# Performance work log

Measured on AMD Instinct MI355X. Metric: run time of the kernel, lower is better.

The kernel has to match this reference:

```python
import jax, jax.numpy as jnp
import numpy as np

B, T, D, H, C = 32, 512, 768, 512, 7


def setup_inputs() -> dict:
    key = jax.random.key(0)
    ks = jax.random.split(key, 10)
    g = lambda k, shape: jax.random.normal(k, shape, jnp.float32) * 0.02
    return {
        "x": jax.random.normal(ks[0], (B, T, D), jnp.float32),
        # PyTorch LSTM params; b = b_ih + b_hh folded into one bias (same math)
        "Wf_ih": g(ks[1], (4 * H, 2 * D)),
        "Wf_hh": g(ks[2], (4 * H, H)),
        "bf": jnp.zeros((4 * H,), jnp.float32),
        "Wb_ih": g(ks[3], (4 * H, 2 * D)),
        "Wb_hh": g(ks[4], (4 * H, H)),
        "bb": jnp.zeros((4 * H,), jnp.float32),
        "W_enc": g(ks[5], (H, D)),
        "b_enc": jnp.zeros((H,), jnp.float32),
        "W_dec": g(ks[6], (H, H)),
        "b_dec": jnp.zeros((H,), jnp.float32),
        "v": jax.random.uniform(ks[7], (H,), jnpp := jnp.float32) if False else jax.random.uniform(ks[7], (H,), jnp.float32),
        "W_head": g(ks[8], (C, 2 * H)),
        "b_head": jnp.zeros((C,), jnp.float32),
    }


def reference(x, Wf_ih, Wf_hh, bf, Wb_ih, Wb_hh, bb, W_enc, b_enc, W_dec, b_dec, v, W_head, b_head):
    hid = W_dec.shape[0]
    # encoder projection is time-invariant -> hoist out of the loop (same math as original)
    enc_proj = jnp.einsum('btd,hd->bth', x, W_enc) + b_enc  # (B,T,H)

    def run_direction(x_seq, Wih, Whh, b):
        def step(carry, xt):
            h, c = carry                                    # (B,H) each
            dec = h @ W_dec.T + b_dec                       # (B,H)
            scores = jnp.tanh(enc_proj + dec[:, None, :]) @ v  # (B,T)
            w = jax.nn.softmax(scores, axis=1)
            ctx = jnp.einsum('bt,btd->bd', w, x)            # (B,D)
            inp = jnp.concatenate([ctx, xt], axis=1)        # (B,2D)
            gates = inp @ Wih.T + h @ Whh.T + b             # (B,4H), torch order i,f,g,o
            i_, f_, g_, o_ = jnp.split(gates, 4, axis=1)
            c = jax.nn.sigmoid(f_) * c + jax.nn.sigmoid(i_) * jnp.tanh(g_)
            h = jax.nn.sigmoid(o_) * jnp.tanh(c)
            return (h, c), h

        h0 = jnp.zeros((x.shape[0], hid), x.dtype)
        (_, _), hs = jax.lax.scan(step, (h0, h0), x_seq)
        return hs                                           # (T,B,H)

    x_seq = jnp.swapaxes(x, 0, 1)                           # (T,B,D)
    hs_f = run_direction(x_seq, Wf_ih, Wf_hh, bf)
    hs_b = run_direction(x_seq[::-1], Wb_ih, Wb_hh, bb)[::-1]
    comb = jnp.swapaxes(jnp.concatenate([hs_f, hs_b], axis=-1), 0, 1)  # (B,T,2H)
    return comb @ W_head.T + b_head                          # (B,T,C)
```

## Files before the change

kernel.cpp:

```cpp
#include <hip/hip_runtime.h>
#include <cstdint>
#include <cstddef>

#define L2E 1.4426950408889634f

typedef __attribute__((ext_vector_type(8))) short short8v;
typedef __attribute__((ext_vector_type(4))) float f32x4;
typedef unsigned long long ull;

__device__ __forceinline__ float fexp2(float x){ return __builtin_amdgcn_exp2f(x); }
__device__ __forceinline__ float frcp(float x){ return __builtin_amdgcn_rcpf(x); }
__device__ __forceinline__ float tanh_f(float x){
  return 1.f - 2.f*frcp(1.f + fexp2(2.f*L2E*x));
}
__device__ __forceinline__ float sigm_f(float x){
  return frcp(1.f + fexp2(-L2E*x));
}
__device__ __forceinline__ float bf2f(ushort u){ return __uint_as_float(((uint32_t)u)<<16); }
__device__ __forceinline__ ushort f2bf(float f){
  uint32_t x = __float_as_uint(f);
  uint32_t r = (x + 0x7FFFu + ((x>>16)&1u)) >> 16;
  return (ushort)r;
}

__device__ __forceinline__ float ld4f(const float* p){
  return __hip_atomic_load((float*)p, __ATOMIC_RELAXED, __HIP_MEMORY_SCOPE_AGENT);
}
__device__ __forceinline__ void st4f(float* p, float v){
  __hip_atomic_store(p, v, __ATOMIC_RELAXED, __HIP_MEMORY_SCOPE_AGENT);
}
__device__ __forceinline__ void st2h(ushort* p, ushort v){
  __hip_atomic_store(p, v, __ATOMIC_RELAXED, __HIP_MEMORY_SCOPE_AGENT);
}
__device__ __forceinline__ short8v ld16h(const ushort* p){
  union { ull u[2]; short8v s; } c;
  c.u[0] = __hip_atomic_load((ull*)p,     __ATOMIC_RELAXED, __HIP_MEMORY_SCOPE_AGENT);
  c.u[1] = __hip_atomic_load((ull*)(p+4), __ATOMIC_RELAXED, __HIP_MEMORY_SCOPE_AGENT);
  return c.s;
}
__device__ __forceinline__ void st8u(ushort* p, ull v){
  __hip_atomic_store((ull*)p, v, __ATOMIC_RELAXED, __HIP_MEMORY_SCOPE_AGENT);
}

namespace {
constexpr int NB = 32, TT = 512, DD = 768, HH = 512;
constexpr size_t EPB  = 0;
constexpr size_t XBB  = EPB  + (size_t)NB*HH*TT*2;
constexpr size_t HSB  = XBB  + (size_t)NB*TT*DD*2;
constexpr size_t WPKB = HSB  + (size_t)2*TT*NB*HH*2;
constexpr size_t WDPB = WPKB + (size_t)2*128*64*64*8*2;
constexpr size_t UCTXB= WDPB + (size_t)32*16*64*8*2;
constexpr size_t ZBB  = UCTXB+ (size_t)2*NB*DD*4;
constexpr size_t DECB = ZBB  + (size_t)2*NB*4;
constexpr size_t CSTB = DECB + (size_t)2*NB*HH*4;
constexpr size_t GSYB = CSTB + (size_t)2*NB*HH*4;
constexpr size_t WS_BYTES = GSYB + 32768;

constexpr int EPL  = 0;
constexpr int WPL  = 65536;
constexpr int REDL = 131072;
constexpr int HEVL = 147456;
constexpr int DPL  = 151552;
constexpr int DECL = 153600;
constexpr int VVL  = 154112;
constexpr int CSCL = 154368;
constexpr int GFNL = 157440;
constexpr int LDS_BYTES = GFNL + 2176;
}

__device__ __forceinline__ void bar_arrive(uint* flags, uint token, int bid){
  __syncthreads();
  if (threadIdx.x == 0)
    __hip_atomic_store(&flags[bid*16], token, __ATOMIC_RELAXED, __HIP_MEMORY_SCOPE_AGENT);
}
__device__ __forceinline__ void bar_wait(uint* flags, uint token){
  if (threadIdx.x < 64) {
    #pragma unroll
    for (int j = 0; j < 4; j++) {
      while (__hip_atomic_load(&flags[(threadIdx.x*4 + j)*16], __ATOMIC_RELAXED, __HIP_MEMORY_SCOPE_AGENT) < token)
        __builtin_amdgcn_s_sleep(1);
    }
  }
  __syncthreads();
  asm volatile("" ::: "memory");
}

__global__ void k_xcast(const float* __restrict__ x, ushort* __restrict__ xb)
{
  size_t i = ((size_t)blockIdx.x*256 + threadIdx.x)*8;
  float4 v0 = *(const float4*)(x + i);
  float4 v1 = *(const float4*)(x + i + 4);
  short8v o;
  o[0]=(short)f2bf(v0.x); o[1]=(short)f2bf(v0.y); o[2]=(short)f2bf(v0.z); o[3]=(short)f2bf(v0.w);
  o[4]=(short)f2bf(v1.x); o[5]=(short)f2bf(v1.y); o[6]=(short)f2bf(v1.z); o[7]=(short)f2bf(v1.w);
  *(short8v*)(xb + i) = o;
}

__global__ void k_encproj(const float* __restrict__ x, const float* __restrict__ Wenc,
                          const float* __restrict__ benc, ushort* __restrict__ epT)
{
  int b = blockIdx.z, h0 = blockIdx.y*64, t0 = blockIdx.x*64;
  __shared__ float As[64][33];
  __shared__ float Bs[64][33];
  int tid = threadIdx.x;
  int n = tid & 63, mg = tid >> 6;
  float acc[16];
  #pragma unroll
  for (int j = 0; j < 16; j++) acc[j] = 0.f;
  int lr = tid >> 2, lk = (tid & 3) * 8;
  for (int k0 = 0; k0 < 768; k0 += 32) {
    const float* ap = Wenc + (size_t)(h0 + lr)*768 + k0 + lk;
    #pragma unroll
    for (int i = 0; i < 8; i++) As[lr][lk + i] = ap[i];
    const float* bp = x + ((size_t)b*512 + t0 + lr)*768 + k0 + lk;
    #pragma unroll
    for (int i = 0; i < 8; i++) Bs[lr][lk + i] = bp[i];
    __syncthreads();
    #pragma unroll
    for (int kk = 0; kk < 32; kk++) {
      float bv = Bs[n][kk];
      #pragma unroll
      for (int j = 0; j < 16; j++) acc[j] += As[mg*16 + j][kk] * bv;
    }
    __syncthreads();
  }
  #pragma unroll
  for (int j = 0; j < 16; j++) {
    int h = h0 + mg*16 + j;
    epT[((size_t)b*512 + h)*512 + t0 + n] = f2bf(acc[j] + benc[h]);
  }
}

__global__ void k_wpack(const float* __restrict__ Wfih, const float* __restrict__ Wfhh,
                        const float* __restrict__ Wbih, const float* __restrict__ Wbhh,
                        ushort* __restrict__ wpk)
{
  size_t f = (size_t)blockIdx.x*256 + threadIdx.x;
  int lane = (int)(f & 63), kstep = (int)((f>>6)&63), jblk = (int)((f>>12)&127), dir = (int)(f>>19);
  const float* Whh = dir ? Wbhh : Wfhh;
  const float* Wih = dir ? Wbih : Wfih;
  int c = lane & 15, gate = c >> 2, jj = c & 3;
  int row = gate*512 + jblk*4 + jj;
  int kbase = kstep*32 + (lane>>4)*8;
  short8v o;
  #pragma unroll
  for (int i = 0; i < 8; i++) {
    int k = kbase + i;
    float w = (k < 512) ? Whh[(size_t)row*512 + k] : Wih[(size_t)row*1536 + (k - 512)];
    o[i] = (short)f2bf(w);
  }
  *(short8v*)(wpk + f*8) = o;
}

__global__ void k_wdpack(const float* __restrict__ Wdec, ushort* __restrict__ wdp)
{
  int f = blockIdx.x*256 + threadIdx.x;
  int lane = f & 63, kstep = (f >> 6) & 15, nb = f >> 10;
  int n = nb*16 + (lane & 15);
  int kbase = kstep*32 + (lane >> 4)*8;
  short8v o;
  #pragma unroll
  for (int i = 0; i < 8; i++) o[i] = (short)f2bf(Wdec[(size_t)n*512 + kbase + i]);
  *(short8v*)(wdp + (size_t)f*8) = o;
}

__device__ __forceinline__ void gates_hx(int s, int wid, int lane, int l15, int lk8, int dirG,
    const ushort* __restrict__ hsb, const ushort* __restrict__ xb,
    const ushort* wpk_l, float* RED)
{
  if (wid >= 2 && wid <= 4) return;
  int b0 = l15, b1 = 16 + l15;
  f32x4 acc0 = {0,0,0,0}, acc1 = {0,0,0,0};
  if (wid < 2) {
    if (s > 0) {
      int t_prev = dirG ? (512 - s) : (s - 1);
      const ushort* h0 = hsb + (((size_t)dirG*512 + t_prev)*32 + b0)*512;
      const ushort* h1 = hsb + (((size_t)dirG*512 + t_prev)*32 + b1)*512;
      #pragma unroll
      for (int kk = 0; kk < 8; kk++) {
        int kstep = wid*8 + kk;
        int ko = kstep*32 + lk8;
        short8v a0v = ld16h(h0 + ko);
        short8v a1v = ld16h(h1 + ko);
        short8v bv  = *(const short8v*)(wpk_l + (size_t)kstep*512 + lane*8);
        acc0 = __builtin_amdgcn_mfma_f32_16x16x32_bf16(a0v, bv, acc0, 0, 0, 0);
        acc1 = __builtin_amdgcn_mfma_f32_16x16x32_bf16(a1v, bv, acc1, 0, 0, 0);
      }
    }
  } else {
    int t_in = dirG ? (511 - s) : s;
    const ushort* x0 = xb + ((size_t)b0*512 + t_in)*768;
    const ushort* x1 = xb + ((size_t)b1*512 + t_in)*768;
    #pragma unroll
    for (int kk = 0; kk < 8; kk++) {
      int kstep = wid*8 + kk;
      int ko = kstep*32 - 1280 + lk8;
      short8v a0v = __builtin_nontemporal_load((const short8v*)(x0 + ko));
      short8v a1v = __builtin_nontemporal_load((const short8v*)(x1 + ko));
      short8v bv  = *(const short8v*)(wpk_l + (size_t)kstep*512 + lane*8);
      acc0 = __builtin_amdgcn_mfma_f32_16x16x32_bf16(a0v, bv, acc0, 0, 0, 0);
      acc1 = __builtin_amdgcn_mfma_f32_16x16x32_bf16(a1v, bv, acc1, 0, 0, 0);
    }
  }
  int rr = (lane >> 4) * 4;
  #pragma unroll
  for (int r = 0; r < 4; r++) RED[((size_t)wid*32 + rr + r)*16 + l15] = acc0[r];
  #pragma unroll
  for (int r = 0; r < 4; r++) RED[((size_t)wid*32 + 16 + rr + r)*16 + l15] = acc1[r];
}

__global__ __launch_bounds__(512, 1) void k_loop(
    ushort* __restrict__ hsb, const ushort* __restrict__ xb, const ushort* __restrict__ ep,
    const ushort* __restrict__ wpk, const ushort* __restrict__ wdp,
    float* __restrict__ spart, ushort* __restrict__ ctxf,
    float* __restrict__ cst, const float* __restrict__ bdec, const float* __restrict__ vg,
    const float* __restrict__ bfv, const float* __restrict__ bbv,
    uint* __restrict__ flags, uint* __restrict__ gfl)
{
  extern __shared__ __align__(16) char dsm[];
  ushort* ep_l  = (ushort*)(dsm + EPL);
  ushort* wpk_l = (ushort*)(dsm + WPL);
  float*  RED   = (float*)(dsm + REDL);
  float*  HEV   = (float*)(dsm + HEVL);
  float*  DP    = (float*)(dsm + DPL);
  float*  DEC   = (float*)(dsm + DECL);
  float*  VV    = (float*)(dsm + VVL);
  float*  CSC   = (float*)(dsm + CSCL);
  float*  GFIN  = (float*)(dsm + GFNL);

  const int bid = blockIdx.x;
  const int tid = threadIdx.x;
  const int wid = tid >> 6, lane = tid & 63;
  const int l15 = lane & 15, lk8 = (lane >> 4) * 8;
  const int bS = bid >> 3, hc = bid & 7;
  const int dirG = bid >> 7, jblkG = bid & 127;
  uint bar_t = 0;

  {
    const short8v* esrc = (const short8v*)(ep + ((size_t)bS*512 + hc*64)*512);
    short8v* edst = (short8v*)ep_l;
    for (int i = tid; i < 4096; i += 512) edst[i] = esrc[i];
    const short8v* wsrc = (const short8v*)(wpk + (((size_t)dirG*128 + jblkG)*64)*512);
    short8v* wdst = (short8v*)wpk_l;
    for (int i = tid; i < 4096; i += 512) wdst[i] = wsrc[i];
    if (tid < 64) VV[tid] = vg[hc*64 + tid];
  }
  ++bar_t; bar_arrive(flags, bar_t, bid); bar_wait(flags, bar_t);

  for (int s = 0; s < TT; ++s) {
    if (s == 0) {
      if (tid < 128) { int dir = tid >> 6, n = tid & 63; DEC[dir*64 + n] = bdec[hc*64 + n]; }
    } else {
      if (tid < 128) {
        int dir = tid >> 6, q = tid & 63;
        int tp = dir ? (512 - s) : (s - 1);
        short8v hv = ld16h(hsb + (((size_t)dir*512 + tp)*32 + bS)*512 + q*8);
        #pragma unroll
        for (int j = 0; j < 8; j++) HEV[dir*512 + q*8 + j] = bf2f((ushort)hv[j]);
      }
      __syncthreads();
      {
        int dir = tid >> 8, n = (tid >> 2) & 63, kq = tid & 3;
        int ng = hc*64 + n;
        int nb = ng >> 4, c = ng & 15;
        const float* hrow = HEV + dir*512 + kq*128;
        float a = 0.f;
        #pragma unroll
        for (int ch = 0; ch < 16; ch++) {
          int kstep = kq*4 + (ch >> 2);
          int lhi = ch & 3;
          short8v w8 = *(const short8v*)(wdp + (((size_t)nb*16 + kstep)*64 + lhi*16 + c)*8);
          #pragma unroll
          for (int j = 0; j < 8; j++) a += bf2f((ushort)w8[j]) * hrow[ch*8 + j];
        }
        DP[tid] = a;
      }
      __syncthreads();
      if (tid < 128) {
        int dir = tid >> 6, n = tid & 63;
        const float* dp = DP + dir*256 + n*4;
        DEC[dir*64 + n] = dp[0] + dp[1] + dp[2] + dp[3] + bdec[hc*64 + n];
      }
    }
    __syncthreads();

    {
      int t = tid;
      float s0 = 0.f, s1 = 0.f;
      #pragma unroll 8
      for (int h = 0; h < 64; h++) {
        float e = bf2f(ep_l[h*512 + t]);
        float vv = VV[h];
        s0 += tanh_f(e + DEC[h]) * vv;
        s1 += tanh_f(e + DEC[64 + h]) * vv;
      }
      float* sp = spart + (((size_t)(bS*8 + hc))*2)*512;
      st4f(sp + t, s0);
      st4f(sp + 512 + t, s1);
    }
    __syncthreads();
    if (tid == 0)
      __hip_atomic_store(&gfl[bid*16], (uint)(s + 1), __ATOMIC_RELAXED, __HIP_MEMORY_SCOPE_AGENT);
    if (tid < 8) {
      while (__hip_atomic_load(&gfl[(bS*8 + tid)*16], __ATOMIC_RELAXED, __HIP_MEMORY_SCOPE_AGENT) < (uint)(s + 1))
        __builtin_amdgcn_s_sleep(1);
    }
    __syncthreads();

    {
      int t = tid;
      float s0 = 0.f, s1 = 0.f;
      #pragma unroll
      for (int j = 0; j < 8; j++) {
        const float* sp = spart + (((size_t)(bS*8 + j))*2)*512;
        s0 += ld4f(sp + t);
        s1 += ld4f(sp + 512 + t);
      }
      s0 = fminf(s0, 100.f); s1 = fminf(s1, 100.f);
      float e0 = fexp2((s0 - 32.f)*L2E);
      float e1 = fexp2((s1 - 32.f)*L2E);
      HEV[t] = e0; HEV[512 + t] = e1;
      float z0 = e0, z1 = e1;
      #pragma unroll
      for (int off = 32; off; off >>= 1) { z0 += __shfl_xor(z0, off); z1 += __shfl_xor(z1, off); }
      if (lane == 0) { DP[wid] = z0; DP[8 + wid] = z1; }
    }
    __syncthreads();
    if (tid < 2) {
      float z = 0.f;
      const float* zp = DP + tid*8;
      #pragma unroll
      for (int w = 0; w < 8; w++) z += zp[w];
      DP[128 + tid] = frcp(z);
    }
    __syncthreads();

    if (tid < 384) {
      int dl = tid % 96, tq = tid / 96;
      const ushort* xp = xb + (((size_t)bS*512 + tq*128)*768) + hc*96 + dl;
      float a0 = 0.f, a1 = 0.f;
      #pragma unroll 8
      for (int t2 = 0; t2 < 128; t2++) {
        float xv = bf2f(xp[(size_t)t2*768]);
        a0 += HEV[tq*128 + t2]*xv;
        a1 += HEV[512 + tq*128 + t2]*xv;
      }
      CSC[(dl*2 + 0)*4 + tq] = a0;
      CSC[(dl*2 + 1)*4 + tq] = a1;
    }
    __syncthreads();
    if (tid < 192) {
      int dl = tid % 96, dir = tid / 96;
      const float* cp = CSC + (dl*2 + dir)*4;
      float cv = (cp[0] + cp[1] + cp[2] + cp[3]) * DP[128 + dir];
      st2h(ctxf + ((size_t)dir*32 + bS)*768 + hc*96 + dl, f2bf(cv));
    }

    ++bar_t; bar_arrive(flags, bar_t, bid);
    gates_hx(s, wid, lane, l15, lk8, dirG, hsb, xb, wpk_l, RED);
    bar_wait(flags, bar_t);

    {
      if (wid >= 2 && wid <= 4) {
        int b0 = l15, b1 = 16 + l15;
        f32x4 acc0 = {0,0,0,0}, acc1 = {0,0,0,0};
        const ushort* c0 = ctxf + ((size_t)dirG*32 + b0)*768;
        const ushort* c1 = ctxf + ((size_t)dirG*32 + b1)*768;
        #pragma unroll
        for (int kk = 0; kk < 8; kk++) {
          int kstep = wid*8 + kk;
          int ko = kstep*32 - 512 + lk8;
          short8v a0v = ld16h(c0 + ko);
          short8v a1v = ld16h(c1 + ko);
          short8v bv  = *(const short8v*)(wpk_l + (size_t)kstep*512 + lane*8);
          acc0 = __builtin_amdgcn_mfma_f32_16x16x32_bf16(a0v, bv, acc0, 0, 0, 0);
          acc1 = __builtin_amdgcn_mfma_f32_16x16x32_bf16(a1v, bv, acc1, 0, 0, 0);
        }
        int rr = (lane >> 4) * 4;
        #pragma unroll
        for (int r = 0; r < 4; r++) RED[((size_t)wid*32 + rr + r)*16 + l15] = acc0[r];
        #pragma unroll
        for (int r = 0; r < 4; r++) RED[((size_t)wid*32 + 16 + rr + r)*16 + l15] = acc1[r];
      }
      __syncthreads();
      {
        int bb = tid >> 4, c = tid & 15;
        float g = 0.f;
        #pragma unroll
        for (int w = 0; w < 8; w++) g += RED[((size_t)w*32 + bb)*16 + c];
        GFIN[bb*17 + c] = g;
      }
      __syncthreads();
      if (tid < 32) {
        int b = tid;
        int j0 = jblkG*4;
        const float* bias = dirG ? bbv : bfv;
        size_t ci0 = ((size_t)dirG*32 + b)*512 + j0;
        float4 co = *(const float4*)&cst[ci0];
        float cold[4] = {co.x, co.y, co.z, co.w};
        float4 cn4;
        ull hp = 0;
        #pragma unroll
        for (int jj = 0; jj < 4; jj++) {
          int j = j0 + jj;
          float gi  = GFIN[b*17 + jj]       + bias[j];
          float gf  = GFIN[b*17 + 4 + jj]   + bias[512 + j];
          float gg  = GFIN[b*17 + 8 + jj]   + bias[1024 + j];
          float go_ = GFIN[b*17 + 12 + jj]  + bias[1536 + j];
          float cn = sigm_f(gf)*cold[jj] + sigm_f(gi)*tanh_f(gg);
          float h  = sigm_f(go_)*tanh_f(cn);
          ((float*)&cn4)[jj] = cn;
          hp |= ((ull)f2bf(h)) << (16*jj);
        }
        *(float4*)&cst[ci0] = cn4;
        int tw = dirG ? (511 - s) : s;
        st8u(hsb + (((size_t)dirG*512 + tw)*32 + b)*512 + j0, hp);
      }
    }
    ++bar_t; bar_arrive(flags, bar_t, bid);
    bar_wait(flags, bar_t);
  }
}

__global__ void k_head(const ushort* __restrict__ hsb, const float* __restrict__ Wh,
                       const float* __restrict__ bh, float* __restrict__ out)
{
  int wid = threadIdx.x >> 6, lane = threadIdx.x & 63;
  int r = blockIdx.x*4 + wid;
  int b = r >> 9, t = r & 511;
  float acc[7];
  #pragma unroll
  for (int c = 0; c < 7; c++) acc[c] = 0.f;
  const ushort* hf = hsb + (((size_t)t)*32 + b)*512;
  const ushort* hb = hsb + (((size_t)512 + t)*32 + b)*512;
  for (int k0 = 0; k0 < 512; k0 += 64) {
    int k = k0 + lane;
    float a = bf2f(hf[k]), bvv = bf2f(hb[k]);
    #pragma unroll
    for (int c = 0; c < 7; c++)
      acc[c] += a*Wh[c*1024 + k] + bvv*Wh[c*1024 + 512 + k];
  }
  #pragma unroll
  for (int c = 0; c < 7; c++) {
    float sres = acc[c];
    #pragma unroll
    for (int off = 32; off; off >>= 1) sres += __shfl_xor(sres, off);
    if (lane == c) out[((size_t)b*512 + t)*7 + c] = sres + bh[c];
  }
}

extern "C" void kernel_launch(void* const* d_in, const int* in_sizes, int n_in,
                              void* d_out, int out_size, void* d_ws, size_t ws_size,
                              hipStream_t stream) {
  (void)in_sizes; (void)n_in; (void)out_size;
  const float* x    = (const float*)d_in[0];
  const float* Wfih = (const float*)d_in[1];
  const float* Wfhh = (const float*)d_in[2];
  const float* bfv  = (const float*)d_in[3];
  const float* Wbih = (const float*)d_in[4];
  const float* Wbhh = (const float*)d_in[5];
  const float* bbv  = (const float*)d_in[6];
  const float* Wenc = (const float*)d_in[7];
  const float* benc = (const float*)d_in[8];
  const float* Wdec = (const float*)d_in[9];
  const float* bdec = (const float*)d_in[10];
  const float* v    = (const float*)d_in[11];
  const float* Whead= (const float*)d_in[12];
  const float* bhead= (const float*)d_in[13];
  float* out = (float*)d_out;
  char* ws = (char*)d_ws;

  if (ws_size < WS_BYTES) return;

  ushort* ep   = (ushort*)(ws + EPB);
  float*  spart= (float*)(ws + EPB);
  ushort* xb   = (ushort*)(ws + XBB);
  ushort* hsb  = (ushort*)(ws + HSB);
  ushort* wpk  = (ushort*)(ws + WPKB);
  ushort* wdp  = (ushort*)(ws + WDPB);
  ushort* ctxf = (ushort*)(ws + UCTXB);
  float*  cst  = (float*)(ws + CSTB);
  uint*   flags= (uint*)(ws + GSYB);
  uint*   gfl  = (uint*)(ws + GSYB + 16384);

  hipFuncSetAttribute(reinterpret_cast<const void*>(k_loop),
                      hipFuncAttributeMaxDynamicSharedMemorySize, LDS_BYTES);

  hipMemsetAsync(ws + CSTB, 0, (size_t)2*NB*HH*4, stream);
  hipMemsetAsync(ws + GSYB, 0, 32768, stream);

  hipLaunchKernelGGL(k_xcast, dim3(6144), dim3(256), 0, stream, x, xb);
  hipLaunchKernelGGL(k_encproj, dim3(8,8,32), dim3(256), 0, stream, x, Wenc, benc, ep);
  hipLaunchKernelGGL(k_wpack, dim3(4096), dim3(256), 0, stream, Wfih, Wfhh, Wbih, Wbhh, wpk);
  hipLaunchKernelGGL(k_wdpack, dim3(128), dim3(256), 0, stream, Wdec, wdp);

  void* args[] = {
    (void*)&hsb, (void*)&xb, (void*)&ep, (void*)&wpk, (void*)&wdp,
    (void*)&spart, (void*)&ctxf, (void*)&cst,
    (void*)&bdec, (void*)&v, (void*)&bfv, (void*)&bbv, (void*)&flags, (void*)&gfl
  };
  hipLaunchCooperativeKernel(reinterpret_cast<void*>(k_loop), dim3(256), dim3(512),
                             args, LDS_BYTES, stream);

  hipLaunchKernelGGL(k_head, dim3(4096), dim3(256), 0, stream, hsb, Whead, bhead, out);
}
```

Measured before the change: 16.11 ms.

## Centralize softmax in leader block and overlap gates_hx with softmax wait

Instead of every block of a batch group gathering all partial scores and computing the softmax redundantly, only the hc==0 block reduces the partials, normalizes, and publishes the weights through a new global buffer and flag. The other blocks run their input-gate MFMA work (gates_hx) while they wait for that flag, which hides part of the cross-block synchronization latency. Several smaller changes come with it: the hidden state is staged as bf16 in padded LDS, the LDS arrays get padded layouts to avoid bank conflicts, the context normalization is folded into the weights, and the barrier wait polls the 256 flags with 256 threads instead of 64 threads each checking four. The cost is an extra global round trip and a dependency on the leader block, which may now sit on the critical path of each step.

```diff
diff --git a/kernel.cpp b/kernel.cpp
--- a/kernel.cpp
+++ b/kernel.cpp
@@ -49,22 +49,22 @@
 constexpr size_t HSB  = XBB  + (size_t)NB*TT*DD*2;
 constexpr size_t WPKB = HSB  + (size_t)2*TT*NB*HH*2;
 constexpr size_t WDPB = WPKB + (size_t)2*128*64*64*8*2;
-constexpr size_t UCTXB= WDPB + (size_t)32*16*64*8*2;
-constexpr size_t ZBB  = UCTXB+ (size_t)2*NB*DD*4;
-constexpr size_t DECB = ZBB  + (size_t)2*NB*4;
-constexpr size_t CSTB = DECB + (size_t)2*NB*HH*4;
+constexpr size_t CTXB = WDPB + (size_t)32*16*64*8*2;
+constexpr size_t EVGB = CTXB + (size_t)2*NB*DD*4;
+constexpr size_t CSTB = EVGB + (size_t)NB*2*512*4;
 constexpr size_t GSYB = CSTB + (size_t)2*NB*HH*4;
-constexpr size_t WS_BYTES = GSYB + 32768;
+constexpr size_t WS_BYTES = GSYB + 49152;
 
 constexpr int EPL  = 0;
 constexpr int WPL  = 65536;
 constexpr int REDL = 131072;
 constexpr int HEVL = 147456;
-constexpr int DPL  = 151552;
-constexpr int DECL = 153600;
-constexpr int VVL  = 154112;
-constexpr int CSCL = 154368;
-constexpr int GFNL = 157440;
+constexpr int HBL  = 151680;
+constexpr int DPL  = 153856;
+constexpr int DECL = 155904;
+constexpr int VVL  = 156416;
+constexpr int CSCL = 156672;
+constexpr int GFNL = 159776;
 constexpr int LDS_BYTES = GFNL + 2176;
 }
 
@@ -74,12 +74,9 @@
     __hip_atomic_store(&flags[bid*16], token, __ATOMIC_RELAXED, __HIP_MEMORY_SCOPE_AGENT);
 }
 __device__ __forceinline__ void bar_wait(uint* flags, uint token){
-  if (threadIdx.x < 64) {
-    #pragma unroll
-    for (int j = 0; j < 4; j++) {
-      while (__hip_atomic_load(&flags[(threadIdx.x*4 + j)*16], __ATOMIC_RELAXED, __HIP_MEMORY_SCOPE_AGENT) < token)
-        __builtin_amdgcn_s_sleep(1);
-    }
+  if (threadIdx.x < 256) {
+    while (__hip_atomic_load(&flags[threadIdx.x*16], __ATOMIC_RELAXED, __HIP_MEMORY_SCOPE_AGENT) < token)
+      __builtin_amdgcn_s_sleep(1);
   }
   __syncthreads();
   asm volatile("" ::: "memory");
@@ -212,16 +209,17 @@
 __global__ __launch_bounds__(512, 1) void k_loop(
     ushort* __restrict__ hsb, const ushort* __restrict__ xb, const ushort* __restrict__ ep,
     const ushort* __restrict__ wpk, const ushort* __restrict__ wdp,
-    float* __restrict__ spart, ushort* __restrict__ ctxf,
+    float* __restrict__ spart, ushort* __restrict__ ctxf, float* __restrict__ evt_g,
     float* __restrict__ cst, const float* __restrict__ bdec, const float* __restrict__ vg,
     const float* __restrict__ bfv, const float* __restrict__ bbv,
-    uint* __restrict__ flags, uint* __restrict__ gfl)
+    uint* __restrict__ flags, uint* __restrict__ gfl, uint* __restrict__ gfl2)
 {
   extern __shared__ __align__(16) char dsm[];
   ushort* ep_l  = (ushort*)(dsm + EPL);
   ushort* wpk_l = (ushort*)(dsm + WPL);
   float*  RED   = (float*)(dsm + REDL);
   float*  HEV   = (float*)(dsm + HEVL);
+  ushort* HB    = (ushort*)(dsm + HBL);
   float*  DP    = (float*)(dsm + DPL);
   float*  DEC   = (float*)(dsm + DECL);
   float*  VV    = (float*)(dsm + VVL);
@@ -255,23 +253,20 @@
         int dir = tid >> 6, q = tid & 63;
         int tp = dir ? (512 - s) : (s - 1);
         short8v hv = ld16h(hsb + (((size_t)dir*512 + tp)*32 + bS)*512 + q*8);
-        #pragma unroll
-        for (int j = 0; j < 8; j++) HEV[dir*512 + q*8 + j] = bf2f((ushort)hv[j]);
+        *(short8v*)&HB[(dir*4 + (q >> 4))*136 + (q & 15)*8] = hv;
       }
       __syncthreads();
       {
         int dir = tid >> 8, n = (tid >> 2) & 63, kq = tid & 3;
-        int ng = hc*64 + n;
-        int nb = ng >> 4, c = ng & 15;
-        const float* hrow = HEV + dir*512 + kq*128;
+        int ng = hc*64 + n, nb = ng >> 4, c = ng & 15;
+        const ushort* hrow = HB + (dir*4 + kq)*136;
         float a = 0.f;
         #pragma unroll
         for (int ch = 0; ch < 16; ch++) {
-          int kstep = kq*4 + (ch >> 2);
-          int lhi = ch & 3;
+          int kstep = kq*4 + (ch >> 2), lhi = ch & 3;
           short8v w8 = *(const short8v*)(wdp + (((size_t)nb*16 + kstep)*64 + lhi*16 + c)*8);
           #pragma unroll
-          for (int j = 0; j < 8; j++) a += bf2f((ushort)w8[j]) * hrow[ch*8 + j];
+          for (int j = 0; j < 8; j++) a += bf2f((ushort)w8[j]) * bf2f(hrow[ch*8 + j]);
         }
         DP[tid] = a;
       }
@@ -284,9 +279,9 @@
     }
     __syncthreads();
 
+    float s0 = 0.f, s1 = 0.f;
     {
       int t = tid;
-      float s0 = 0.f, s1 = 0.f;
       #pragma unroll 8
       for (int h = 0; h < 64; h++) {
         float e = bf2f(ep_l[h*512 + t]);
@@ -294,70 +289,91 @@
         s0 += tanh_f(e + DEC[h]) * vv;
         s1 += tanh_f(e + DEC[64 + h]) * vv;
       }
+    }
+
+    if (hc != 0) {
       float* sp = spart + (((size_t)(bS*8 + hc))*2)*512;
-      st4f(sp + t, s0);
-      st4f(sp + 512 + t, s1);
-    }
-    __syncthreads();
-    if (tid == 0)
-      __hip_atomic_store(&gfl[bid*16], (uint)(s + 1), __ATOMIC_RELAXED, __HIP_MEMORY_SCOPE_AGENT);
-    if (tid < 8) {
-      while (__hip_atomic_load(&gfl[(bS*8 + tid)*16], __ATOMIC_RELAXED, __HIP_MEMORY_SCOPE_AGENT) < (uint)(s + 1))
-        __builtin_amdgcn_s_sleep(1);
-    }
-    __syncthreads();
-
-    {
-      int t = tid;
-      float s0 = 0.f, s1 = 0.f;
+      st4f(sp + tid, s0);
+      st4f(sp + 512 + tid, s1);
+      __syncthreads();
+      if (tid == 0)
+        __hip_atomic_store(&gfl[bid*16], (uint)(s + 1), __ATOMIC_RELAXED, __HIP_MEMORY_SCOPE_AGENT);
+      gates_hx(s, wid, lane, l15, lk8, dirG, hsb, xb, wpk_l, RED);
+      if (tid == 0) {
+        while (__hip_atomic_load(&gfl2[bS*16], __ATOMIC_RELAXED, __HIP_MEMORY_SCOPE_AGENT) < (uint)(s + 1))
+          __builtin_amdgcn_s_sleep(1);
+      }
+      __syncthreads();
+      {
+        float e0 = ld4f(evt_g + (size_t)bS*1024 + tid);
+        float e1 = ld4f(evt_g + (size_t)bS*1024 + 512 + tid);
+        HEV[(tid >> 7)*132 + (tid & 127)] = e0;
+        HEV[(4 + (tid >> 7))*132 + (tid & 127)] = e1;
+      }
+      __syncthreads();
+    } else {
+      if (tid >= 1 && tid < 8) {
+        while (__hip_atomic_load(&gfl[(bS*8 + tid)*16], __ATOMIC_RELAXED, __HIP_MEMORY_SCOPE_AGENT) < (uint)(s + 1))
+          __builtin_amdgcn_s_sleep(1);
+      }
+      __syncthreads();
+      float s0r = s0, s1r = s1;
       #pragma unroll
-      for (int j = 0; j < 8; j++) {
+      for (int j = 1; j < 8; j++) {
         const float* sp = spart + (((size_t)(bS*8 + j))*2)*512;
-        s0 += ld4f(sp + t);
-        s1 += ld4f(sp + 512 + t);
-      }
-      s0 = fminf(s0, 100.f); s1 = fminf(s1, 100.f);
-      float e0 = fexp2((s0 - 32.f)*L2E);
-      float e1 = fexp2((s1 - 32.f)*L2E);
-      HEV[t] = e0; HEV[512 + t] = e1;
+        s0r += ld4f(sp + tid);
+        s1r += ld4f(sp + 512 + tid);
+      }
+      s0r = fminf(s0r, 100.f); s1r = fminf(s1r, 100.f);
+      float e0 = fexp2((s0r - 32.f)*L2E);
+      float e1 = fexp2((s1r - 32.f)*L2E);
       float z0 = e0, z1 = e1;
       #pragma unroll
       for (int off = 32; off; off >>= 1) { z0 += __shfl_xor(z0, off); z1 += __shfl_xor(z1, off); }
       if (lane == 0) { DP[wid] = z0; DP[8 + wid] = z1; }
-    }
-    __syncthreads();
-    if (tid < 2) {
-      float z = 0.f;
-      const float* zp = DP + tid*8;
-      #pragma unroll
-      for (int w = 0; w < 8; w++) z += zp[w];
-      DP[128 + tid] = frcp(z);
-    }
-    __syncthreads();
+      __syncthreads();
+      if (tid < 2) {
+        float z = 0.f;
+        #pragma unroll
+        for (int w = 0; w < 8; w++) z += DP[tid*8 + w];
+        DP[128 + tid] = frcp(z);
+      }
+      __syncthreads();
+      e0 *= DP[128]; e1 *= DP[129];
+      HEV[(tid >> 7)*132 + (tid & 127)] = e0;
+      HEV[(4 + (tid >> 7))*132 + (tid & 127)] = e1;
+      st4f(evt_g + (size_t)bS*1024 + tid, e0);
+      st4f(evt_g + (size_t)bS*1024 + 512 + tid, e1);
+      __syncthreads();
+      if (tid == 0)
+        __hip_atomic_store(&gfl2[bS*16], (uint)(s + 1), __ATOMIC_RELAXED, __HIP_MEMORY_SCOPE_AGENT);
+    }
 
     if (tid < 384) {
       int dl = tid % 96, tq = tid / 96;
       const ushort* xp = xb + (((size_t)bS*512 + tq*128)*768) + hc*96 + dl;
+      const float* ev0 = HEV + tq*132;
+      const float* ev1 = HEV + (4 + tq)*132;
       float a0 = 0.f, a1 = 0.f;
       #pragma unroll 8
       for (int t2 = 0; t2 < 128; t2++) {
         float xv = bf2f(xp[(size_t)t2*768]);
-        a0 += HEV[tq*128 + t2]*xv;
-        a1 += HEV[512 + tq*128 + t2]*xv;
-      }
-      CSC[(dl*2 + 0)*4 + tq] = a0;
-      CSC[(dl*2 + 1)*4 + tq] = a1;
+        a0 += ev0[t2]*xv;
+        a1 += ev1[t2]*xv;
+      }
+      CSC[(tq*2 + 0)*97 + dl] = a0;
+      CSC[(tq*2 + 1)*97 + dl] = a1;
     }
     __syncthreads();
     if (tid < 192) {
       int dl = tid % 96, dir = tid / 96;
-      const float* cp = CSC + (dl*2 + dir)*4;
-      float cv = (cp[0] + cp[1] + cp[2] + cp[3]) * DP[128 + dir];
+      float cv = CSC[(0*2 + dir)*97 + dl] + CSC[(1*2 + dir)*97 + dl]
+               + CSC[(2*2 + dir)*97 + dl] + CSC[(3*2 + dir)*97 + dl];
       st2h(ctxf + ((size_t)dir*32 + bS)*768 + hc*96 + dl, f2bf(cv));
     }
 
     ++bar_t; bar_arrive(flags, bar_t, bid);
-    gates_hx(s, wid, lane, l15, lk8, dirG, hsb, xb, wpk_l, RED);
+    if (hc == 0) gates_hx(s, wid, lane, l15, lk8, dirG, hsb, xb, wpk_l, RED);
     bar_wait(flags, bar_t);
 
     {
@@ -478,16 +494,18 @@
   ushort* hsb  = (ushort*)(ws + HSB);
   ushort* wpk  = (ushort*)(ws + WPKB);
   ushort* wdp  = (ushort*)(ws + WDPB);
-  ushort* ctxf = (ushort*)(ws + UCTXB);
+  ushort* ctxf = (ushort*)(ws + CTXB);
+  float*  evtg = (float*)(ws + EVGB);
   float*  cst  = (float*)(ws + CSTB);
   uint*   flags= (uint*)(ws + GSYB);
   uint*   gfl  = (uint*)(ws + GSYB + 16384);
+  uint*   gfl2 = (uint*)(ws + GSYB + 32768);
 
   hipFuncSetAttribute(reinterpret_cast<const void*>(k_loop),
                       hipFuncAttributeMaxDynamicSharedMemorySize, LDS_BYTES);
 
   hipMemsetAsync(ws + CSTB, 0, (size_t)2*NB*HH*4, stream);
-  hipMemsetAsync(ws + GSYB, 0, 32768, stream);
+  hipMemsetAsync(ws + GSYB, 0, 49152, stream);
 
   hipLaunchKernelGGL(k_xcast, dim3(6144), dim3(256), 0, stream, x, xb);
   hipLaunchKernelGGL(k_encproj, dim3(8,8,32), dim3(256), 0, stream, x, Wenc, benc, ep);
@@ -496,8 +514,9 @@
 
   void* args[] = {
     (void*)&hsb, (void*)&xb, (void*)&ep, (void*)&wpk, (void*)&wdp,
-    (void*)&spart, (void*)&ctxf, (void*)&cst,
-    (void*)&bdec, (void*)&v, (void*)&bfv, (void*)&bbv, (void*)&flags, (void*)&gfl
+    (void*)&spart, (void*)&ctxf, (void*)&evtg, (void*)&cst,
+    (void*)&bdec, (void*)&v, (void*)&bfv, (void*)&bbv,
+    (void*)&flags, (void*)&gfl, (void*)&gfl2
   };
   hipLaunchCooperativeKernel(reinterpret_cast<void*>(k_loop), dim3(256), dim3(512),
                              args, LDS_BYTES, stream);
```

Measured after the change: 14.77 ms. 8.3% less time.
